# Kernel tuning notes

Hardware: AMD Instinct MI355X
Metric: run time of the kernel (lower is better)

## Reference

```python
import jax, jax.numpy as jnp
import numpy as np

B, N, F_DIM, R_DIM = 4, 512, 64, 128


def _pair_indices(n):
    # Same order as the original python double loop: i outer, j inner, skip i==j.
    ii, jj = np.meshgrid(np.arange(n), np.arange(n), indexing='ij')
    mask = ii != jj
    return jnp.asarray(ii[mask]), jnp.asarray(jj[mask])  # each [N*(N-1)]


def setup_inputs() -> dict:
    key = jax.random.key(0)
    ks = jax.random.split(key, 7)
    s1 = 1.0 / np.sqrt(2 * F_DIM)
    s2 = 1.0 / np.sqrt(R_DIM)
    return {
        'features': jax.random.normal(ks[0], (B, N, F_DIM), dtype=jnp.float32),
        'W1': jax.random.uniform(ks[1], (2 * F_DIM, R_DIM), jnp.float32, -s1, s1),
        'b1': jax.random.uniform(ks[2], (R_DIM,), jnp.float32, -s1, s1),
        'W2': jax.random.uniform(ks[3], (R_DIM, R_DIM), jnp.float32, -s2, s2),
        'b2': jax.random.uniform(ks[4], (R_DIM,), jnp.float32, -s2, s2),
        'W3': jax.random.uniform(ks[5], (R_DIM, 1), jnp.float32, -s2, s2),
        'b3': jax.random.uniform(ks[6], (1,), jnp.float32, -s2, s2),
    }


def reference(features, W1, b1, W2, b2, W3, b3):
    n = features.shape[1]
    idx_i, idx_j = _pair_indices(n)
    # Gather all ordered pairs (i != j): [B, P, 2F]
    pair = jnp.concatenate([features[:, idx_i, :], features[:, idx_j, :]], axis=-1)
    h = jax.nn.relu(jnp.einsum('bpf,fr->bpr', pair, W1) + b1)
    h = jax.nn.relu(jnp.einsum('bpr,rs->bps', h, W2) + b2)
    out = jnp.einsum('bpr,ro->bpo', h, W3) + b3  # [B, P, 1]
    return out
```

## Files before the change

### kernel.cpp

```cpp
#include <hip/hip_runtime.h>
#include <stdint.h>

#define B_ 4
#define N_ 512
#define F_ 64
#define R_ 128
#define PPI 511
#define TJ 128
#define VSTR 136

typedef _Float16 f16x8 __attribute__((ext_vector_type(8)));
typedef _Float16 f16x2 __attribute__((ext_vector_type(2)));
typedef float f32x4 __attribute__((ext_vector_type(4)));

__device__ __forceinline__ uint16_t f16bits(float x) {
  return __builtin_bit_cast(uint16_t, (_Float16)x);
}
__device__ __forceinline__ f16x2 cvt_pk(float a, float b) {
  return __builtin_bit_cast(f16x2, __builtin_amdgcn_cvt_pkrtz(a, b));
}

__global__ __launch_bounds__(256) void prep_all(
    const float* __restrict__ feat, const float* __restrict__ W1,
    const float* __restrict__ b1, const float* __restrict__ W2,
    uint16_t* __restrict__ U, uint16_t* __restrict__ V, uint16_t* __restrict__ w2f) {
  if (blockIdx.x >= 512) {
    const int d = (blockIdx.x - 512) * 256 + threadIdx.x;
    const int jj = d & 7, lane = (d >> 3) & 63, tc = d >> 9;
    const int c = tc & 3, t = tc >> 2;
    const int rr = 32 * c + (lane >> 4) * 8 + jj;
    const int s = 16 * t + (lane & 15);
    w2f[d] = f16bits(W2[rr * R_ + s]);
    return;
  }
  __shared__ float fs[4][F_];
  const int row0 = blockIdx.x * 4;
  const int tid = threadIdx.x;
  if (tid < 4 * F_) fs[tid >> 6][tid & 63] = feat[row0 * F_ + tid];
  __syncthreads();
  const int r = tid & 127, rh = tid >> 7;
  float aU[2], aV[2];
  const float bias = b1[r];
#pragma unroll
  for (int ii = 0; ii < 2; ++ii) { aU[ii] = bias; aV[ii] = 0.f; }
#pragma unroll 8
  for (int f = 0; f < F_; ++f) {
    const float wa = W1[f * R_ + r];
    const float wb = W1[(F_ + f) * R_ + r];
#pragma unroll
    for (int ii = 0; ii < 2; ++ii) {
      aU[ii] = fmaf(fs[rh * 2 + ii][f], wa, aU[ii]);
      aV[ii] = fmaf(fs[rh * 2 + ii][f], wb, aV[ii]);
    }
  }
#pragma unroll
  for (int ii = 0; ii < 2; ++ii) {
    const int row = row0 + rh * 2 + ii;
    U[row * R_ + r] = f16bits(aU[ii]);
    V[row * R_ + r] = f16bits(aV[ii]);
  }
}

__global__ __launch_bounds__(256, 3) void relnet_main(
    const uint16_t* __restrict__ U, const uint16_t* __restrict__ V,
    const uint16_t* __restrict__ w2f, const float* __restrict__ b2,
    const float* __restrict__ W3, const float* __restrict__ b3,
    float* __restrict__ out) {
  __shared__ __align__(16) uint16_t Vs[TJ * VSTR];
  __shared__ float pl[4][2][2][8][16];

  const int bid = blockIdx.x;
  const int jb = bid & 3, ib = (bid >> 2) & 255, b = bid >> 10;
  const int i0 = ib * 2, j0 = jb * TJ;
  const int tid = threadIdx.x;

  {
    const uint4* sv = (const uint4*)(V + (b * N_ + j0) * R_);
    for (int l = tid; l < TJ * 16; l += 256) {
      const int row = l >> 4, seg = l & 15;
      *(uint4*)&Vs[row * VSTR + seg * 8] = sv[row * 16 + seg];
    }
  }

  const int lane = tid & 63, wave = tid >> 6;
  const int quad = lane >> 4, l4 = lane & 15;
  const int il = wave >> 1, th = wave & 1;
  const int i = i0 + il;

  f16x8 w2r[4][4];
#pragma unroll
  for (int tp = 0; tp < 4; ++tp)
#pragma unroll
    for (int c = 0; c < 4; ++c) {
      const int t = th * 4 + tp;
      const uint4 w = *(const uint4*)(w2f + ((size_t)((t * 4 + c) * 64 + lane)) * 8);
      w2r[tp][c] = __builtin_bit_cast(f16x8, w);
    }

  f32x4 b2f[4];
  f16x2 w3p[4][2];
#pragma unroll
  for (int tp = 0; tp < 4; ++tp) {
    const int s0 = 16 * (th * 4 + tp) + 4 * quad;
    b2f[tp] = (f32x4){b2[s0], b2[s0 + 1], b2[s0 + 2], b2[s0 + 3]};
    w3p[tp][0] = (f16x2){(_Float16)W3[s0], (_Float16)W3[s0 + 1]};
    w3p[tp][1] = (f16x2){(_Float16)W3[s0 + 2], (_Float16)W3[s0 + 3]};
  }

  f16x8 uf[4];
#pragma unroll
  for (int c = 0; c < 4; ++c)
    uf[c] = __builtin_bit_cast(f16x8,
        *(const uint4*)(U + (size_t)(b * N_ + i) * R_ + c * 32 + quad * 8));

  const f16x8 z8 = {};
  const f16x2 z2 = {};

  __syncthreads();

#pragma unroll
  for (int jt = 0; jt < 8; ++jt) {
    f16x8 hb[4];
#pragma unroll
    for (int c = 0; c < 4; ++c) {
      const uint4 v = *(const uint4*)&Vs[(jt * 16 + l4) * VSTR + c * 32 + quad * 8];
      hb[c] = __builtin_elementwise_max(__builtin_bit_cast(f16x8, v) + uf[c], z8);
    }

    f32x4 acc[4];
#pragma unroll
    for (int tp = 0; tp < 4; ++tp) acc[tp] = b2f[tp];
#pragma unroll
    for (int c = 0; c < 4; ++c)
#pragma unroll
      for (int tp = 0; tp < 4; ++tp)
        acc[tp] = __builtin_amdgcn_mfma_f32_16x16x32_f16(w2r[tp][c], hb[c], acc[tp], 0, 0, 0);

    float t0 = 0.f, t1 = 0.f, t2 = 0.f, t3 = 0.f;
#pragma unroll
    for (int tp = 0; tp < 4; tp += 2) {
      f16x2 p0 = __builtin_elementwise_max(cvt_pk(acc[tp][0], acc[tp][1]), z2);
      f16x2 p1 = __builtin_elementwise_max(cvt_pk(acc[tp][2], acc[tp][3]), z2);
      t0 = __builtin_amdgcn_fdot2(p0, w3p[tp][0], t0, false);
      t1 = __builtin_amdgcn_fdot2(p1, w3p[tp][1], t1, false);
      f16x2 q0 = __builtin_elementwise_max(cvt_pk(acc[tp + 1][0], acc[tp + 1][1]), z2);
      f16x2 q1 = __builtin_elementwise_max(cvt_pk(acc[tp + 1][2], acc[tp + 1][3]), z2);
      t2 = __builtin_amdgcn_fdot2(q0, w3p[tp + 1][0], t2, false);
      t3 = __builtin_amdgcn_fdot2(q1, w3p[tp + 1][1], t3, false);
    }
    pl[quad][th][il][jt][l4] = (t0 + t1) + (t2 + t3);
  }

  __syncthreads();

  {
    const int ril = tid >> 7, rjt = (tid >> 4) & 7, rl4 = tid & 15;
    float sum = b3[0];
#pragma unroll
    for (int q = 0; q < 4; ++q)
#pragma unroll
      for (int h = 0; h < 2; ++h) sum += pl[q][h][ril][rjt][rl4];
    const int ri = i0 + ril;
    const int j = j0 + rjt * 16 + rl4;
    if (j != ri) {
      const int p = (b * N_ + ri) * PPI + (j < ri ? j : j - 1);
      out[p] = sum;
    }
  }
}

extern "C" void kernel_launch(void* const* d_in, const int* in_sizes, int n_in,
                              void* d_out, int out_size, void* d_ws, size_t ws_size,
                              hipStream_t stream) {
  const float* feat = (const float*)d_in[0];
  const float* W1 = (const float*)d_in[1];
  const float* b1 = (const float*)d_in[2];
  const float* W2 = (const float*)d_in[3];
  const float* b2 = (const float*)d_in[4];
  const float* W3 = (const float*)d_in[5];
  const float* b3 = (const float*)d_in[6];

  uint16_t* U = (uint16_t*)d_ws;
  uint16_t* V = U + (size_t)B_ * N_ * R_;
  uint16_t* w2f = V + (size_t)B_ * N_ * R_;

  prep_all<<<512 + 64, 256, 0, stream>>>(feat, W1, b1, W2, U, V, w2f);
  relnet_main<<<B_ * (N_ / 2) * (N_ / TJ), 256, 0, stream>>>(U, V, w2f, b2, W3, b3,
                                                             (float*)d_out);
}
```

Measured before the change: 105.5 us.

## Give each wave a full i row and all W2 tiles, four i per block

Each wave now owns one i row and computes all eight 16-column output tiles of layer 2, so W2 fragments are held entirely in registers per wave instead of being split across two waves. Each block covers four i rows instead of two, so every V tile staged in shared memory is reused by twice as many rows and the grid is halved. The partial-sum scratch is laid out per wave with padding, and layer-3 reduction is interleaved per tile. The cost is much higher register pressure (occupancy hint lowered from 3 to 2 blocks), which may reduce latency hiding.

```diff
diff --git a/kernel.cpp b/kernel.cpp
--- a/kernel.cpp
+++ b/kernel.cpp
@@ -61,17 +61,17 @@
   }
 }
 
-__global__ __launch_bounds__(256, 3) void relnet_main(
+__global__ __launch_bounds__(256, 2) void relnet_main(
     const uint16_t* __restrict__ U, const uint16_t* __restrict__ V,
     const uint16_t* __restrict__ w2f, const float* __restrict__ b2,
     const float* __restrict__ W3, const float* __restrict__ b3,
     float* __restrict__ out) {
   __shared__ __align__(16) uint16_t Vs[TJ * VSTR];
-  __shared__ float pl[4][2][2][8][16];
+  __shared__ float pl[4][8][4][17];
 
   const int bid = blockIdx.x;
-  const int jb = bid & 3, ib = (bid >> 2) & 255, b = bid >> 10;
-  const int i0 = ib * 2, j0 = jb * TJ;
+  const int jb = bid & 3, ib = (bid >> 2) & 127, b = bid >> 9;
+  const int i0 = ib * 4, j0 = jb * TJ;
   const int tid = threadIdx.x;
 
   {
@@ -84,27 +84,26 @@
 
   const int lane = tid & 63, wave = tid >> 6;
   const int quad = lane >> 4, l4 = lane & 15;
-  const int il = wave >> 1, th = wave & 1;
+  const int il = wave;
   const int i = i0 + il;
 
-  f16x8 w2r[4][4];
+  f16x8 w2r[8][4];
 #pragma unroll
-  for (int tp = 0; tp < 4; ++tp)
+  for (int t = 0; t < 8; ++t)
 #pragma unroll
     for (int c = 0; c < 4; ++c) {
-      const int t = th * 4 + tp;
       const uint4 w = *(const uint4*)(w2f + ((size_t)((t * 4 + c) * 64 + lane)) * 8);
-      w2r[tp][c] = __builtin_bit_cast(f16x8, w);
+      w2r[t][c] = __builtin_bit_cast(f16x8, w);
     }
 
-  f32x4 b2f[4];
-  f16x2 w3p[4][2];
+  f32x4 b2f[8];
+  f16x2 w3p[8][2];
 #pragma unroll
-  for (int tp = 0; tp < 4; ++tp) {
-    const int s0 = 16 * (th * 4 + tp) + 4 * quad;
-    b2f[tp] = (f32x4){b2[s0], b2[s0 + 1], b2[s0 + 2], b2[s0 + 3]};
-    w3p[tp][0] = (f16x2){(_Float16)W3[s0], (_Float16)W3[s0 + 1]};
-    w3p[tp][1] = (f16x2){(_Float16)W3[s0 + 2], (_Float16)W3[s0 + 3]};
+  for (int t = 0; t < 8; ++t) {
+    const int s0 = 16 * t + 4 * quad;
+    b2f[t] = (f32x4){b2[s0], b2[s0 + 1], b2[s0 + 2], b2[s0 + 3]};
+    w3p[t][0] = (f16x2){(_Float16)W3[s0], (_Float16)W3[s0 + 1]};
+    w3p[t][1] = (f16x2){(_Float16)W3[s0 + 2], (_Float16)W3[s0 + 3]};
   }
 
   f16x8 uf[4];
@@ -127,41 +126,36 @@
       hb[c] = __builtin_elementwise_max(__builtin_bit_cast(f16x8, v) + uf[c], z8);
     }
 
-    f32x4 acc[4];
+    float sA = 0.f, sB = 0.f, sC = 0.f, sD = 0.f;
 #pragma unroll
-    for (int tp = 0; tp < 4; ++tp) acc[tp] = b2f[tp];
+    for (int t = 0; t < 8; ++t) {
+      f32x4 acc = __builtin_amdgcn_mfma_f32_16x16x32_f16(w2r[t][0], hb[0], b2f[t], 0, 0, 0);
 #pragma unroll
-    for (int c = 0; c < 4; ++c)
-#pragma unroll
-      for (int tp = 0; tp < 4; ++tp)
-        acc[tp] = __builtin_amdgcn_mfma_f32_16x16x32_f16(w2r[tp][c], hb[c], acc[tp], 0, 0, 0);
-
-    float t0 = 0.f, t1 = 0.f, t2 = 0.f, t3 = 0.f;
-#pragma unroll
-    for (int tp = 0; tp < 4; tp += 2) {
-      f16x2 p0 = __builtin_elementwise_max(cvt_pk(acc[tp][0], acc[tp][1]), z2);
-      f16x2 p1 = __builtin_elementwise_max(cvt_pk(acc[tp][2], acc[tp][3]), z2);
-      t0 = __builtin_amdgcn_fdot2(p0, w3p[tp][0], t0, false);
-      t1 = __builtin_amdgcn_fdot2(p1, w3p[tp][1], t1, false);
-      f16x2 q0 = __builtin_elementwise_max(cvt_pk(acc[tp + 1][0], acc[tp + 1][1]), z2);
-      f16x2 q1 = __builtin_elementwise_max(cvt_pk(acc[tp + 1][2], acc[tp + 1][3]), z2);
-      t2 = __builtin_amdgcn_fdot2(q0, w3p[tp + 1][0], t2, false);
-      t3 = __builtin_amdgcn_fdot2(q1, w3p[tp + 1][1], t3, false);
+      for (int c = 1; c < 4; ++c)
+        acc = __builtin_amdgcn_mfma_f32_16x16x32_f16(w2r[t][c], hb[c], acc, 0, 0, 0);
+      const f16x2 p0 = __builtin_elementwise_max(cvt_pk(acc[0], acc[1]), z2);
+      const f16x2 p1 = __builtin_elementwise_max(cvt_pk(acc[2], acc[3]), z2);
+      if (t & 1) {
+        sC = __builtin_amdgcn_fdot2(p0, w3p[t][0], sC, false);
+        sD = __builtin_amdgcn_fdot2(p1, w3p[t][1], sD, false);
+      } else {
+        sA = __builtin_amdgcn_fdot2(p0, w3p[t][0], sA, false);
+        sB = __builtin_amdgcn_fdot2(p1, w3p[t][1], sB, false);
+      }
     }
-    pl[quad][th][il][jt][l4] = (t0 + t1) + (t2 + t3);
+    pl[il][jt][quad][l4] = (sA + sC) + (sB + sD);
   }
 
   __syncthreads();
 
-  {
-    const int ril = tid >> 7, rjt = (tid >> 4) & 7, rl4 = tid & 15;
-    float sum = b3[0];
 #pragma unroll
-    for (int q = 0; q < 4; ++q)
-#pragma unroll
-      for (int h = 0; h < 2; ++h) sum += pl[q][h][ril][rjt][rl4];
-    const int ri = i0 + ril;
-    const int j = j0 + rjt * 16 + rl4;
+  for (int ro = 0; ro < 2; ++ro) {
+    const int idx = tid + ro * 256;
+    const int til = idx >> 7, tjt = (idx >> 4) & 7, tl4 = idx & 15;
+    const float sum = b3[0] + ((pl[til][tjt][0][tl4] + pl[til][tjt][1][tl4]) +
+                               (pl[til][tjt][2][tl4] + pl[til][tjt][3][tl4]));
+    const int ri = i0 + til;
+    const int j = j0 + tjt * 16 + tl4;
     if (j != ri) {
       const int p = (b * N_ + ri) * PPI + (j < ri ? j : j - 1);
       out[p] = sum;
@@ -185,6 +179,6 @@
   uint16_t* w2f = V + (size_t)B_ * N_ * R_;
 
   prep_all<<<512 + 64, 256, 0, stream>>>(feat, W1, b1, W2, U, V, w2f);
-  relnet_main<<<B_ * (N_ / 2) * (N_ / TJ), 256, 0, stream>>>(U, V, w2f, b2, W3, b3,
+  relnet_main<<<B_ * (N_ / 4) * (N_ / TJ), 256, 0, stream>>>(U, V, w2f, b2, W3, b3,
                                                              (float*)d_out);
 }
```

After: 109.0 us. 1.03x slower.
